# Kernel tuning notes

Hardware: AMD Instinct MI355X
Metric: run time of the kernel (lower is better)

## Reference

```python
import jax, jax.numpy as jnp
import numpy as np

B, S, H, NH = 2, 2048, 1024, 16
D = H // NH  # per-head dim = 64
NEG = -1000000000.0
EPS = 1e-6


def setup_inputs() -> dict:
    key = jax.random.key(0)
    ks = jax.random.split(key, 8)
    q = jax.random.normal(ks[0], (B, S, H), dtype=jnp.float32)
    k = jax.random.normal(ks[1], (B, S, H), dtype=jnp.float32)
    v = jax.random.normal(ks[2], (B, S, H), dtype=jnp.float32)
    mask = jax.random.randint(ks[3], (B, S, S), 0, 2, dtype=jnp.int32)
    # learned params (torch Linear stores W as [out,in]; y = x @ W.T)
    sc = 1.0 / np.sqrt(H)
    Wq = jax.random.normal(ks[4], (H, H), dtype=jnp.float32) * sc
    Wk = jax.random.normal(ks[5], (H, H), dtype=jnp.float32) * sc
    Wv = jax.random.normal(ks[6], (H, H), dtype=jnp.float32) * sc
    ln_gamma = jnp.ones((H,), dtype=jnp.float32)
    ln_beta = jnp.zeros((H,), dtype=jnp.float32)
    return {"q": q, "k": k, "v": v, "mask": mask,
            "Wq": Wq, "Wk": Wk, "Wv": Wv,
            "ln_gamma": ln_gamma, "ln_beta": ln_beta}


def _mha(q, k, v, mask, Wq, Wk, Wv, ln_gamma, ln_beta):
    residual = q
    # projections: note original never applies self.scale, and self.fc is unused
    qh = (q @ Wq.T).reshape(B, S, NH, D).transpose(0, 2, 1, 3)  # [B,NH,S,D]
    kh = (k @ Wk.T).reshape(B, S, NH, D).transpose(0, 2, 1, 3)
    vh = (v @ Wv.T).reshape(B, S, NH, D).transpose(0, 2, 1, 3)
    scores = jnp.einsum('bhqd,bhkd->bhqk', qh, kh)  # NO 1/sqrt(d) scaling (faithful)
    scores = jnp.where(mask[:, None, :, :] == 0, NEG, scores)
    attn = jax.nn.softmax(scores, axis=-1)
    ctx = jnp.einsum('bhqk,bhkd->bhqd', attn, vh)
    ctx = ctx.transpose(0, 2, 1, 3).reshape(B, S, H)
    ctx = ctx + residual  # dropout = identity in eval
    mu = jnp.mean(ctx, axis=-1, keepdims=True)
    var = jnp.var(ctx, axis=-1, keepdims=True)
    out = (ctx - mu) / jnp.sqrt(var + EPS) * ln_gamma + ln_beta
    return out, attn


def reference(q, k, v, mask, Wq, Wk, Wv, ln_gamma, ln_beta):
    return _mha(q, k, v, mask, Wq, Wk, Wv, ln_gamma, ln_beta)
```

## Files before the change

kernel.cpp:

```cpp
#include <hip/hip_runtime.h>
#include <hip/hip_fp16.h>

typedef _Float16 f16;
typedef _Float16 f16x8 __attribute__((ext_vector_type(8)));
typedef _Float16 f16x4 __attribute__((ext_vector_type(4)));
typedef float    f32x4 __attribute__((ext_vector_type(4)));
typedef float    f32x2 __attribute__((ext_vector_type(2)));

#define NEGV -1000000000.0f

#define BAR_LDS() asm volatile("s_waitcnt lgkmcnt(0)\n\ts_barrier" ::: "memory")

__global__ __launch_bounds__(256) void cvt3(const float* __restrict__ a,
                                            const float* __restrict__ b,
                                            const float* __restrict__ c,
                                            f16* __restrict__ out, int per) {
  const float* src = blockIdx.y == 0 ? a : (blockIdx.y == 1 ? b : c);
  int i = (blockIdx.x * 256 + threadIdx.x) * 4;
  if (i >= per) return;
  f32x4 v = *(const f32x4*)(src + i);
  f16x4 h; h[0]=(f16)v[0]; h[1]=(f16)v[1]; h[2]=(f16)v[2]; h[3]=(f16)v[3];
  *(f16x4*)(out + (size_t)blockIdx.y * per + i) = h;
}

__global__ __launch_bounds__(256) void pack_mask(const int* __restrict__ m,
                                                 unsigned* __restrict__ bits) {
  size_t i = (size_t)blockIdx.x * 256 + threadIdx.x;
  unsigned long long b = __ballot(m[i] != 0);
  int lane = threadIdx.x & 63;
  if (lane == 0)       bits[i >> 5] = (unsigned)b;
  else if (lane == 32) bits[i >> 5] = (unsigned)(b >> 32);
}

__device__ inline void gld16(const void* g, void* l) {
  __builtin_amdgcn_global_load_lds((const __attribute__((address_space(1))) void*)g,
                                   (__attribute__((address_space(3))) void*)l, 16, 0, 0);
}

__global__ __launch_bounds__(256) void gemm_proj(const f16* __restrict__ Xall,
                                                 const f16* __restrict__ Wall,
                                                 f16* __restrict__ Qh,
                                                 f16* __restrict__ Kh,
                                                 f16* __restrict__ Vn) {
  __shared__ f16 lA[4][128][8];
  __shared__ f16 lB[4][128][8];
  const int z = blockIdx.z;
  const f16* A  = Xall + (size_t)z * (4096u * 1024u);
  const f16* Wt = Wall + (size_t)z * (1024u * 1024u);
  f16* Y = (z == 0) ? Qh : (z == 1 ? Kh : Vn);
  const int t = threadIdx.x;
  const int brow = blockIdx.y * 128, bcol = blockIdx.x * 128;
  const int w = t >> 6, l = t & 63;
  const int wr = w >> 1, wc = w & 1;
  const int lr = l & 15, lg = l >> 4;
  f32x4 acc[4][4] = {};

  for (int k0 = 0; k0 < 1024; k0 += 32) {
#pragma unroll
    for (int j = 0; j < 2; j++) {
      const int p = j * 4096 + t * 16;
      const int ks = p >> 11, row = (p >> 4) & 127;
      gld16(A  + (size_t)(brow + row) * 1024 + k0 + ks * 8, (char*)lA + p);
      gld16(Wt + (size_t)(bcol + row) * 1024 + k0 + ks * 8, (char*)lB + p);
    }
    __syncthreads();
    f16x8 af[4], bf[4];
#pragma unroll
    for (int mi = 0; mi < 4; mi++) af[mi] = *(const f16x8*)&lA[lg][wr * 64 + mi * 16 + lr][0];
#pragma unroll
    for (int ni = 0; ni < 4; ni++) bf[ni] = *(const f16x8*)&lB[lg][wc * 64 + ni * 16 + lr][0];
#pragma unroll
    for (int mi = 0; mi < 4; mi++)
#pragma unroll
      for (int ni = 0; ni < 4; ni++)
        acc[mi][ni] = __builtin_amdgcn_mfma_f32_16x16x32_f16(af[mi], bf[ni], acc[mi][ni], 0, 0, 0);
    __syncthreads();
  }

  const int mb0 = brow + wr * 64, nb0 = bcol + wc * 64;
#pragma unroll
  for (int mi = 0; mi < 4; mi++)
#pragma unroll
    for (int ni = 0; ni < 4; ni++)
#pragma unroll
      for (int j = 0; j < 4; j++) {
        const int m = mb0 + mi * 16 + lg * 4 + j;
        const int n = nb0 + ni * 16 + lr;
        const int bb = m >> 11, s = m & 2047;
        const int h = n >> 6, d = n & 63;
        Y[((((size_t)bb * 16 + h) * 2048 + s) << 6) + d] = (f16)acc[mi][ni][j];
      }
}

__global__ __launch_bounds__(512) void transposeV(const f16* __restrict__ Vn,
                                                  f16* __restrict__ VhT) {
  const int bh = blockIdx.y, s0 = blockIdx.x * 64;
  const int t = threadIdx.x, l = t & 63, w = t >> 6;
  const f16x8 v = *(const f16x8*)(Vn + (((size_t)bh * 2048 + s0 + l) << 6) + w * 8);
#pragma unroll
  for (int e = 0; e < 8; e++)
    VhT[(((size_t)bh * 64 + w * 8 + e) << 11) + s0 + l] = v[e];
}

__global__ __launch_bounds__(512, 4) void sumexp_k(const f16* __restrict__ Qh,
                                                   const f16* __restrict__ Kh,
                                                   const unsigned* __restrict__ mbits,
                                                   float* __restrict__ SIo) {
  __shared__ f16 lK[8][128][8];
  const int wg = blockIdx.x;
  const int bh = ((wg & 7) << 2) | (wg >> 7);
  const int qg = (wg >> 3) & 15;
  const int b = bh >> 4;
  const int t = threadIdx.x, w = t >> 6, l = t & 63;
  const int lr = l & 15, lg = l >> 4;
  const int qr = qg * 128 + w * 16;

  const int pA = t * 16, pB = 8192 + t * 16;
  const int ksA = pA >> 11, rwA = (pA >> 4) & 127;
  const int ksB = pB >> 11, rwB = (pB >> 4) & 127;
  const f16* Kbase = Kh + ((size_t)bh << 17);

  const f16* qp = Qh + (((size_t)bh * 2048 + qr + lr) << 6) + lg * 8;
  const f16x8 aq0 = *(const f16x8*)qp;
  const f16x8 aq1 = *(const f16x8*)(qp + 32);
  const unsigned* mrow0 = mbits + ((size_t)b * 2048 + qr + lg * 4) * 64;

  float sj[4] = {0.f, 0.f, 0.f, 0.f};
  f16x8 kra = *(const f16x8*)(Kbase + ((size_t)rwA << 6) + ksA * 8);
  f16x8 krb = *(const f16x8*)(Kbase + ((size_t)rwB << 6) + ksB * 8);
  for (int t16 = 0; t16 < 16; t16++) {
    const int kb = t16 * 128;
    BAR_LDS();
    *(f16x8*)((char*)lK + pA) = kra;
    *(f16x8*)((char*)lK + pB) = krb;
    BAR_LDS();
    uint4 mrow[4];
#pragma unroll
    for (int j = 0; j < 4; j++) mrow[j] = *(const uint4*)(mrow0 + j * 64 + (kb >> 5));
    if (t16 < 15) {
      const f16* nb = Kbase + ((size_t)(kb + 128) << 6);
      kra = *(const f16x8*)(nb + ((size_t)rwA << 6) + ksA * 8);
      krb = *(const f16x8*)(nb + ((size_t)rwB << 6) + ksB * 8);
    }
#pragma unroll
    for (int nf = 0; nf < 8; nf++) {
      f32x4 s4 = {};
      s4 = __builtin_amdgcn_mfma_f32_16x16x32_f16(aq0, *(const f16x8*)&lK[lg][nf * 16 + lr][0], s4, 0, 0, 0);
      s4 = __builtin_amdgcn_mfma_f32_16x16x32_f16(aq1, *(const f16x8*)&lK[4 + lg][nf * 16 + lr][0], s4, 0, 0, 0);
      const unsigned bp = ((nf & 1) << 4) + lr;
#pragma unroll
      for (int j = 0; j < 4; j++) {
        const unsigned bit = (((const unsigned*)&mrow[j])[nf >> 1] >> bp) & 1u;
        sj[j] += bit ? __expf(s4[j]) : 0.f;
      }
    }
  }
#pragma unroll
  for (int j = 0; j < 4; j++) {
#pragma unroll
    for (int o = 1; o < 16; o <<= 1) sj[j] += __shfl_xor(sj[j], o, 64);
  }
  if (lr == 0) {
    float* o = SIo + ((size_t)bh << 11) + qr + lg * 4;
    o[0] = 1.0f / sj[0]; o[1] = 1.0f / sj[1];
    o[2] = 1.0f / sj[2]; o[3] = 1.0f / sj[3];
  }
}

__device__ inline char* swzW(char* wb, int row, int col) {
  return wb + row * 256 + ((col * 2) ^ ((row & 7) << 4));
}

__global__ __launch_bounds__(512, 4) void attn_pv(const f16* __restrict__ Qh,
                                                  const f16* __restrict__ Kh,
                                                  const f16* __restrict__ VhT,
                                                  const unsigned* __restrict__ mbits,
                                                  const float* __restrict__ SIo,
                                                  float* __restrict__ attn,
                                                  float* __restrict__ ctx) {
  __shared__ f16 lK[8][128][8];
  __shared__ f16 lVT[16][64][8];
  __shared__ char Pw[8 * 4096];
  const int wg = blockIdx.x;
  const int bh = ((wg & 7) << 2) | (wg >> 7);
  const int qg = (wg >> 3) & 15;
  const int b = bh >> 4, h = bh & 15;
  const int t = threadIdx.x, w = t >> 6, l = t & 63;
  const int lr = l & 15, lg = l >> 4;
  const int qr = qg * 128 + w * 16;
  char* wb = Pw + w * 4096;

  const int pA = t * 16, pB = 8192 + t * 16;
  const int ksA = pA >> 11, rwA = (pA >> 4) & 127;
  const int ksB = pB >> 11, rwB = (pB >> 4) & 127;
  const int vsA = pA >> 10, vdA = (pA >> 4) & 63;
  const int vsB = pB >> 10, vdB = (pB >> 4) & 63;
  const f16* Kbase = Kh + ((size_t)bh << 17);
  const f16* Vbase = VhT + ((size_t)bh << 17);

  const f16* qp = Qh + (((size_t)bh * 2048 + qr + lr) << 6) + lg * 8;
  const f16x8 aq0 = *(const f16x8*)qp;
  const f16x8 aq1 = *(const f16x8*)(qp + 32);
  const unsigned* mrow0 = mbits + ((size_t)b * 2048 + qr + lg * 4) * 64;

  float SI[4];
#pragma unroll
  for (int j = 0; j < 4; j++) SI[j] = SIo[((size_t)bh << 11) + qr + lg * 4 + j];

  f32x4 acc[4] = {};
  f16x8 kra = *(const f16x8*)(Kbase + ((size_t)rwA << 6) + ksA * 8);
  f16x8 krb = *(const f16x8*)(Kbase + ((size_t)rwB << 6) + ksB * 8);
  f16x8 vra = *(const f16x8*)(Vbase + ((size_t)vdA << 11) + vsA * 8);
  f16x8 vrb = *(const f16x8*)(Vbase + ((size_t)vdB << 11) + vsB * 8);
  float* abase = attn + (((size_t)bh * 2048 + qr) << 11);
  const int srow = l >> 3, scol = (l & 7) * 4;
  for (int t16 = 0; t16 < 16; t16++) {
    const int kb = t16 * 128;
    BAR_LDS();
    *(f16x8*)((char*)lK + pA) = kra;
    *(f16x8*)((char*)lK + pB) = krb;
    *(f16x8*)((char*)lVT + pA) = vra;
    *(f16x8*)((char*)lVT + pB) = vrb;
    BAR_LDS();
    uint4 mrow[4];
#pragma unroll
    for (int j = 0; j < 4; j++) mrow[j] = *(const uint4*)(mrow0 + j * 64 + (kb >> 5));
    if (t16 < 15) {
      const f16* nk = Kbase + ((size_t)(kb + 128) << 6);
      kra = *(const f16x8*)(nk + ((size_t)rwA << 6) + ksA * 8);
      krb = *(const f16x8*)(nk + ((size_t)rwB << 6) + ksB * 8);
      const f16* nv = Vbase + kb + 128;
      vra = *(const f16x8*)(nv + ((size_t)vdA << 11) + vsA * 8);
      vrb = *(const f16x8*)(nv + ((size_t)vdB << 11) + vsB * 8);
    }
#pragma unroll
    for (int nf = 0; nf < 8; nf++) {
      f32x4 s4 = {};
      s4 = __builtin_amdgcn_mfma_f32_16x16x32_f16(aq0, *(const f16x8*)&lK[lg][nf * 16 + lr][0], s4, 0, 0, 0);
      s4 = __builtin_amdgcn_mfma_f32_16x16x32_f16(aq1, *(const f16x8*)&lK[4 + lg][nf * 16 + lr][0], s4, 0, 0, 0);
      const unsigned bp = ((nf & 1) << 4) + lr;
#pragma unroll
      for (int j = 0; j < 4; j++) {
        const unsigned bit = (((const unsigned*)&mrow[j])[nf >> 1] >> bp) & 1u;
        const float pj = bit ? __expf(s4[j]) * SI[j] : 0.f;
        *(f16*)swzW(wb, lg * 4 + j, nf * 16 + lr) = (f16)pj;
      }
    }
#pragma unroll
    for (int kk = 0; kk < 4; kk++) {
      const f16x8 pa = *(const f16x8*)swzW(wb, lr, kk * 32 + lg * 8);
#pragma unroll
      for (int nf = 0; nf < 4; nf++)
        acc[nf] = __builtin_amdgcn_mfma_f32_16x16x32_f16(pa, *(const f16x8*)&lVT[kk * 4 + lg][nf * 16 + lr][0], acc[nf], 0, 0, 0);
    }
#pragma unroll
    for (int h2 = 0; h2 < 2; h2++) {
      const int row = srow + h2 * 8;
      float* arow = abase + ((size_t)row << 11) + kb + scol;
#pragma unroll
      for (int u = 0; u < 4; u++) {
        const f16x4 p4 = *(const f16x4*)swzW(wb, row, scol + u * 32);
        f32x4 o;
#pragma unroll
        for (int e = 0; e < 4; e++) o[e] = (float)p4[e];
        *(f32x4*)(arow + u * 32) = o;
      }
    }
  }

#pragma unroll
  for (int nf = 0; nf < 4; nf++)
#pragma unroll
    for (int j = 0; j < 4; j++)
      ctx[((size_t)b * 2048 + qr + lg * 4 + j) * 1024 + h * 64 + nf * 16 + lr] = acc[nf][j];
}

__global__ __launch_bounds__(256) void ln_res(const float* __restrict__ qres,
                                              const float* __restrict__ gamma,
                                              const float* __restrict__ beta,
                                              float* __restrict__ io) {
  const int tok = blockIdx.x;
  const int t = threadIdx.x;
  float* rowp = io + (size_t)tok * 1024;
  const float* qp = qres + (size_t)tok * 1024;
  const f32x4 c = *(const f32x4*)(rowp + t * 4);
  const f32x4 r = *(const f32x4*)(qp + t * 4);
  f32x4 vals;
  float s = 0.f, s2 = 0.f;
#pragma unroll
  for (int e = 0; e < 4; e++) { float x = c[e] + r[e]; vals[e] = x; s += x; s2 += x * x; }
#pragma unroll
  for (int o = 1; o < 64; o <<= 1) { s += __shfl_xor(s, o, 64); s2 += __shfl_xor(s2, o, 64); }
  __shared__ float rs[4][2];
  const int w = t >> 6;
  if ((t & 63) == 0) { rs[w][0] = s; rs[w][1] = s2; }
  __syncthreads();
  s  = rs[0][0] + rs[1][0] + rs[2][0] + rs[3][0];
  s2 = rs[0][1] + rs[1][1] + rs[2][1] + rs[3][1];
  const float mu = s * (1.f / 1024.f);
  const float var = s2 * (1.f / 1024.f) - mu * mu;
  const float rstd = rsqrtf(var + 1e-6f);
  const f32x4 g  = *(const f32x4*)(gamma + t * 4);
  const f32x4 be = *(const f32x4*)(beta + t * 4);
  f32x4 o;
#pragma unroll
  for (int e = 0; e < 4; e++) o[e] = (vals[e] - mu) * rstd * g[e] + be[e];
  *(f32x4*)(rowp + t * 4) = o;
}

extern "C" void kernel_launch(void* const* d_in, const int* in_sizes, int n_in,
                              void* d_out, int out_size, void* d_ws, size_t ws_size,
                              hipStream_t stream) {
  const float* q     = (const float*)d_in[0];
  const float* k     = (const float*)d_in[1];
  const float* v     = (const float*)d_in[2];
  const int*   mask  = (const int*)d_in[3];
  const float* Wq    = (const float*)d_in[4];
  const float* Wk    = (const float*)d_in[5];
  const float* Wv    = (const float*)d_in[6];
  const float* gamma = (const float*)d_in[7];
  const float* beta  = (const float*)d_in[8];
  float* out  = (float*)d_out;
  float* attn = out + (size_t)4194304;
  const size_t MB = 1u << 20;
  char* ws = (char*)d_ws;

  f16 *x16, *W16, *Qh, *Kh, *Vn, *VhT; unsigned* mb; float* SIo;
  if (ws_size >= 65 * MB) {
    x16 = (f16*)ws;              W16 = (f16*)(ws + 24 * MB);
    Qh  = (f16*)(ws + 30 * MB);  Kh  = (f16*)(ws + 38 * MB);
    Vn  = (f16*)(ws + 46 * MB);  VhT = (f16*)(ws + 54 * MB);
    mb  = (unsigned*)(ws + 62 * MB);
    SIo = (float*)(ws + 63 * MB);
  } else {
    x16 = (f16*)attn;            W16 = (f16*)((char*)attn + 24 * MB);
    Vn  = (f16*)((char*)attn + 30 * MB);
    Qh  = (f16*)ws;              Kh  = (f16*)(ws + 8 * MB);
    VhT = (f16*)(ws + 16 * MB);  mb  = (unsigned*)(ws + 24 * MB);
    SIo = (float*)(ws + 25 * MB);
  }

  cvt3<<<dim3(4096, 3), 256, 0, stream>>>(q, k, v, x16, 4194304);
  cvt3<<<dim3(1024, 3), 256, 0, stream>>>(Wq, Wk, Wv, W16, 1048576);
  pack_mask<<<dim3(32768), 256, 0, stream>>>(mask, mb);
  gemm_proj<<<dim3(8, 32, 3), 256, 0, stream>>>(x16, W16, Qh, Kh, Vn);
  transposeV<<<dim3(32, 32), 512, 0, stream>>>(Vn, VhT);
  sumexp_k<<<dim3(512), 512, 0, stream>>>(Qh, Kh, mb, SIo);
  attn_pv<<<dim3(512), 512, 0, stream>>>(Qh, Kh, VhT, mb, SIo, attn, out);
  ln_res<<<dim3(4096), 256, 0, stream>>>(q, gamma, beta, out);
}
```

Baseline: 309.3 us.

## Transpose score MFMA so each lane owns a query row, write attn directly

The QK^T MFMA operands are swapped so each lane holds four consecutive key columns of one query row. Each lane can then load a single mask uint4 per tile and write the fp32 attention probabilities straight to global memory as f32x4. This removes the second LDS read-back pass that rebuilt fp32 rows from the f16 staging buffer. The f16 copy of P for the PV MFMA is now written as f16x4 vectors instead of scalars. sumexp_k gets the same layout, needs only two shuffles instead of a 16-lane reduction, and raises its occupancy hint to 6. The catch is that global attn stores now have a more scattered pattern: each lane writes 16B pieces spread across 16 rows.

```diff
diff --git a/kernel.cpp b/kernel.cpp
--- a/kernel.cpp
+++ b/kernel.cpp
@@ -5,9 +5,6 @@
 typedef _Float16 f16x8 __attribute__((ext_vector_type(8)));
 typedef _Float16 f16x4 __attribute__((ext_vector_type(4)));
 typedef float    f32x4 __attribute__((ext_vector_type(4)));
-typedef float    f32x2 __attribute__((ext_vector_type(2)));
-
-#define NEGV -1000000000.0f
 
 #define BAR_LDS() asm volatile("s_waitcnt lgkmcnt(0)\n\ts_barrier" ::: "memory")
 
@@ -102,7 +99,8 @@
     VhT[(((size_t)bh * 64 + w * 8 + e) << 11) + s0 + l] = v[e];
 }
 
-__global__ __launch_bounds__(512, 4) void sumexp_k(const f16* __restrict__ Qh,
+
+__global__ __launch_bounds__(512, 6) void sumexp_k(const f16* __restrict__ Qh,
                                                    const f16* __restrict__ Kh,
                                                    const unsigned* __restrict__ mbits,
                                                    float* __restrict__ SIo) {
@@ -123,9 +121,9 @@
   const f16* qp = Qh + (((size_t)bh * 2048 + qr + lr) << 6) + lg * 8;
   const f16x8 aq0 = *(const f16x8*)qp;
   const f16x8 aq1 = *(const f16x8*)(qp + 32);
-  const unsigned* mrow0 = mbits + ((size_t)b * 2048 + qr + lg * 4) * 64;
-
-  float sj[4] = {0.f, 0.f, 0.f, 0.f};
+  const unsigned* mrow = mbits + ((size_t)b * 2048 + qr + lr) * 64;
+
+  float sum = 0.f;
   f16x8 kra = *(const f16x8*)(Kbase + ((size_t)rwA << 6) + ksA * 8);
   f16x8 krb = *(const f16x8*)(Kbase + ((size_t)rwB << 6) + ksB * 8);
   for (int t16 = 0; t16 < 16; t16++) {
@@ -134,9 +132,8 @@
     *(f16x8*)((char*)lK + pA) = kra;
     *(f16x8*)((char*)lK + pB) = krb;
     BAR_LDS();
-    uint4 mrow[4];
-#pragma unroll
-    for (int j = 0; j < 4; j++) mrow[j] = *(const uint4*)(mrow0 + j * 64 + (kb >> 5));
+    const uint4 mw4 = *(const uint4*)(mrow + (kb >> 5));
+    const unsigned mwv[4] = {mw4.x, mw4.y, mw4.z, mw4.w};
     if (t16 < 15) {
       const f16* nb = Kbase + ((size_t)(kb + 128) << 6);
       kra = *(const f16x8*)(nb + ((size_t)rwA << 6) + ksA * 8);
@@ -145,30 +142,18 @@
 #pragma unroll
     for (int nf = 0; nf < 8; nf++) {
       f32x4 s4 = {};
-      s4 = __builtin_amdgcn_mfma_f32_16x16x32_f16(aq0, *(const f16x8*)&lK[lg][nf * 16 + lr][0], s4, 0, 0, 0);
-      s4 = __builtin_amdgcn_mfma_f32_16x16x32_f16(aq1, *(const f16x8*)&lK[4 + lg][nf * 16 + lr][0], s4, 0, 0, 0);
-      const unsigned bp = ((nf & 1) << 4) + lr;
-#pragma unroll
-      for (int j = 0; j < 4; j++) {
-        const unsigned bit = (((const unsigned*)&mrow[j])[nf >> 1] >> bp) & 1u;
-        sj[j] += bit ? __expf(s4[j]) : 0.f;
-      }
+      s4 = __builtin_amdgcn_mfma_f32_16x16x32_f16(*(const f16x8*)&lK[lg][nf * 16 + lr][0], aq0, s4, 0, 0, 0);
+      s4 = __builtin_amdgcn_mfma_f32_16x16x32_f16(*(const f16x8*)&lK[4 + lg][nf * 16 + lr][0], aq1, s4, 0, 0, 0);
+      const unsigned word = mwv[nf >> 1];
+      const unsigned bp = ((nf & 1) << 4) + lg * 4;
+#pragma unroll
+      for (int j = 0; j < 4; j++)
+        sum += ((word >> (bp + j)) & 1u) ? __expf(s4[j]) : 0.f;
     }
   }
-#pragma unroll
-  for (int j = 0; j < 4; j++) {
-#pragma unroll
-    for (int o = 1; o < 16; o <<= 1) sj[j] += __shfl_xor(sj[j], o, 64);
-  }
-  if (lr == 0) {
-    float* o = SIo + ((size_t)bh << 11) + qr + lg * 4;
-    o[0] = 1.0f / sj[0]; o[1] = 1.0f / sj[1];
-    o[2] = 1.0f / sj[2]; o[3] = 1.0f / sj[3];
-  }
-}
-
-__device__ inline char* swzW(char* wb, int row, int col) {
-  return wb + row * 256 + ((col * 2) ^ ((row & 7) << 4));
+  sum += __shfl_xor(sum, 16, 64);
+  sum += __shfl_xor(sum, 32, 64);
+  if (l < 16) SIo[((size_t)bh << 11) + qr + lr] = 1.0f / sum;
 }
 
 __global__ __launch_bounds__(512, 4) void attn_pv(const f16* __restrict__ Qh,
@@ -180,7 +165,7 @@
                                                   float* __restrict__ ctx) {
   __shared__ f16 lK[8][128][8];
   __shared__ f16 lVT[16][64][8];
-  __shared__ char Pw[8 * 4096];
+  __shared__ __align__(16) char Pw[8][4096];
   const int wg = blockIdx.x;
   const int bh = ((wg & 7) << 2) | (wg >> 7);
   const int qg = (wg >> 3) & 15;
@@ -188,7 +173,7 @@
   const int t = threadIdx.x, w = t >> 6, l = t & 63;
   const int lr = l & 15, lg = l >> 4;
   const int qr = qg * 128 + w * 16;
-  char* wb = Pw + w * 4096;
+  char* wb = Pw[w];
 
   const int pA = t * 16, pB = 8192 + t * 16;
   const int ksA = pA >> 11, rwA = (pA >> 4) & 127;
@@ -201,19 +186,17 @@
   const f16* qp = Qh + (((size_t)bh * 2048 + qr + lr) << 6) + lg * 8;
   const f16x8 aq0 = *(const f16x8*)qp;
   const f16x8 aq1 = *(const f16x8*)(qp + 32);
-  const unsigned* mrow0 = mbits + ((size_t)b * 2048 + qr + lg * 4) * 64;
-
-  float SI[4];
-#pragma unroll
-  for (int j = 0; j < 4; j++) SI[j] = SIo[((size_t)bh << 11) + qr + lg * 4 + j];
+  const unsigned* mrow = mbits + ((size_t)b * 2048 + qr + lr) * 64;
+  const float SIq = SIo[((size_t)bh << 11) + qr + lr];
+  float* arow = attn + (((size_t)bh * 2048 + qr + lr) << 11);
 
   f32x4 acc[4] = {};
   f16x8 kra = *(const f16x8*)(Kbase + ((size_t)rwA << 6) + ksA * 8);
   f16x8 krb = *(const f16x8*)(Kbase + ((size_t)rwB << 6) + ksB * 8);
   f16x8 vra = *(const f16x8*)(Vbase + ((size_t)vdA << 11) + vsA * 8);
   f16x8 vrb = *(const f16x8*)(Vbase + ((size_t)vdB << 11) + vsB * 8);
-  float* abase = attn + (((size_t)bh * 2048 + qr) << 11);
-  const int srow = l >> 3, scol = (l & 7) * 4;
+  const int pswz = (lr & 7) << 4;
+
   for (int t16 = 0; t16 < 16; t16++) {
     const int kb = t16 * 128;
     BAR_LDS();
@@ -222,9 +205,8 @@
     *(f16x8*)((char*)lVT + pA) = vra;
     *(f16x8*)((char*)lVT + pB) = vrb;
     BAR_LDS();
-    uint4 mrow[4];
-#pragma unroll
-    for (int j = 0; j < 4; j++) mrow[j] = *(const uint4*)(mrow0 + j * 64 + (kb >> 5));
+    const uint4 mw4 = *(const uint4*)(mrow + (kb >> 5));
+    const unsigned mwv[4] = {mw4.x, mw4.y, mw4.z, mw4.w};
     if (t16 < 15) {
       const f16* nk = Kbase + ((size_t)(kb + 128) << 6);
       kra = *(const f16x8*)(nk + ((size_t)rwA << 6) + ksA * 8);
@@ -236,35 +218,25 @@
 #pragma unroll
     for (int nf = 0; nf < 8; nf++) {
       f32x4 s4 = {};
-      s4 = __builtin_amdgcn_mfma_f32_16x16x32_f16(aq0, *(const f16x8*)&lK[lg][nf * 16 + lr][0], s4, 0, 0, 0);
-      s4 = __builtin_amdgcn_mfma_f32_16x16x32_f16(aq1, *(const f16x8*)&lK[4 + lg][nf * 16 + lr][0], s4, 0, 0, 0);
-      const unsigned bp = ((nf & 1) << 4) + lr;
+      s4 = __builtin_amdgcn_mfma_f32_16x16x32_f16(*(const f16x8*)&lK[lg][nf * 16 + lr][0], aq0, s4, 0, 0, 0);
+      s4 = __builtin_amdgcn_mfma_f32_16x16x32_f16(*(const f16x8*)&lK[4 + lg][nf * 16 + lr][0], aq1, s4, 0, 0, 0);
+      const unsigned word = mwv[nf >> 1];
+      const unsigned bp = ((nf & 1) << 4) + lg * 4;
+      f32x4 po; f16x4 ph;
 #pragma unroll
       for (int j = 0; j < 4; j++) {
-        const unsigned bit = (((const unsigned*)&mrow[j])[nf >> 1] >> bp) & 1u;
-        const float pj = bit ? __expf(s4[j]) * SI[j] : 0.f;
-        *(f16*)swzW(wb, lg * 4 + j, nf * 16 + lr) = (f16)pj;
+        const float pj = ((word >> (bp + j)) & 1u) ? __expf(s4[j]) * SIq : 0.f;
+        po[j] = pj; ph[j] = (f16)pj;
       }
+      *(f32x4*)(arow + kb + nf * 16 + lg * 4) = po;
+      *(f16x4*)(wb + lr * 256 + ((nf * 32 + lg * 8) ^ pswz)) = ph;
     }
 #pragma unroll
     for (int kk = 0; kk < 4; kk++) {
-      const f16x8 pa = *(const f16x8*)swzW(wb, lr, kk * 32 + lg * 8);
+      const f16x8 pa = *(const f16x8*)(wb + lr * 256 + ((kk * 64 + lg * 16) ^ pswz));
 #pragma unroll
       for (int nf = 0; nf < 4; nf++)
         acc[nf] = __builtin_amdgcn_mfma_f32_16x16x32_f16(pa, *(const f16x8*)&lVT[kk * 4 + lg][nf * 16 + lr][0], acc[nf], 0, 0, 0);
-    }
-#pragma unroll
-    for (int h2 = 0; h2 < 2; h2++) {
-      const int row = srow + h2 * 8;
-      float* arow = abase + ((size_t)row << 11) + kb + scol;
-#pragma unroll
-      for (int u = 0; u < 4; u++) {
-        const f16x4 p4 = *(const f16x4*)swzW(wb, row, scol + u * 32);
-        f32x4 o;
-#pragma unroll
-        for (int e = 0; e < 4; e++) o[e] = (float)p4[e];
-        *(f32x4*)(arow + u * 32) = o;
-      }
     }
   }
 
```

Measured after the change: 333.7 us. 1.08x slower.
